# Optimization experiments

Measured on AMD Instinct MI355X. Metric: run time of the kernel, lower is better.

The kernel has to match this reference:

```python
import jax, jax.numpy as jnp
import numpy as np

LN_EPS = 1e-5

def _layernorm(x, gamma, beta):
    mu = jnp.mean(x, axis=-1, keepdims=True)
    var = jnp.var(x, axis=-1, keepdims=True)
    return (x - mu) * jax.lax.rsqrt(var + LN_EPS) * gamma + beta

def setup_inputs() -> dict:
    key = jax.random.key(0)
    ks = jax.random.split(key, 4)
    B, s, d, L = 8, 192, 512, 8
    h = 2048  # embed_dim * 2
    return {
        "lags": jax.random.normal(ks[0], (B, s, d, L), dtype=jnp.float32),
        "gamma1": jnp.ones((d,), jnp.float32),
        "beta1": jnp.zeros((d,), jnp.float32),
        "W1": jax.random.normal(ks[1], (d, h), jnp.float32) * (1.0 / np.sqrt(d)),
        "b1": jnp.zeros((h,), jnp.float32),
        "W2": jax.random.normal(ks[2], (h, d), jnp.float32) * (1.0 / np.sqrt(h)),
        "b2": jnp.zeros((d,), jnp.float32),
        "gamma3": jnp.ones((d,), jnp.float32),
        "beta3": jnp.zeros((d,), jnp.float32),
    }

def reference(lags, gamma1, beta1, W1, b1, W2, b2, gamma3, beta3):
    B, s, d, L = lags.shape
    # (B, s, d, L) -> (B, s, L, d) -> (B, S=s*L, d)
    x = jnp.transpose(lags, (0, 1, 3, 2)).reshape(B, s * L, d)
    scale = 1.0 / jnp.sqrt(jnp.asarray(d, x.dtype))
    # single-head, unprojected attention: scores = X X^T / sqrt(d)
    scores = jnp.einsum('bqd,bkd->bqk', x, x) * scale  # [B, S, S]
    attn = jax.nn.softmax(scores, axis=-1)
    attn_out = jnp.einsum('bqk,bkd->bqd', attn, x)
    q = _layernorm(x + attn_out, gamma1, beta1)
    ff = jnp.dot(jax.nn.gelu(jnp.dot(q, W1) + b1, approximate=False), W2) + b2
    out = _layernorm(q + ff, gamma3, beta3)
    # (B, S, d) -> (B, s, L, d) -> (B, s, d, L)
    return jnp.transpose(out.reshape(B, s, L, d), (0, 1, 3, 2))
```

## Files before the change

### kernel.cpp

```cpp
#include <hip/hip_runtime.h>
#include <hip/hip_bf16.h>
#include <math.h>

#define B_ 8
#define S_ 192
#define D_ 512
#define L_ 8
#define SQ 1536
#define H_ 2048
#define NROW (B_*SQ)
#define SCALE_QK 0.04419417382415922f
#define SCALE_QK2 0.06377551974755906f

typedef unsigned short ushort_t;
typedef unsigned int uint_t;
typedef __attribute__((ext_vector_type(8))) short bf16x8;
typedef __attribute__((ext_vector_type(4))) float f32x4;

__device__ __forceinline__ float bfu2f(ushort_t u) { return __uint_as_float((unsigned)u << 16); }
__device__ __forceinline__ ushort_t f2bfu(float f) {
  __hip_bfloat16 h = __float2bfloat16(f);
  return *reinterpret_cast<ushort_t*>(&h);
}

__device__ __forceinline__ float gelu_tanh(float x) {
  float x2 = x * x;
  float u2 = x * fmaf(0.0713548162f, x2, 1.5957691216f);
  float e = __expf(u2);
  float r = fmaf(-2.0f, __builtin_amdgcn_rcpf(e + 1.0f), 1.0f);
  float hx = 0.5f * x;
  return fmaf(hx, r, hx);
}

__device__ __forceinline__ void gl_lds16(const ushort_t* g, ushort_t* l) {
  __builtin_amdgcn_global_load_lds(
      (const __attribute__((address_space(1))) unsigned int*)g,
      (__attribute__((address_space(3))) unsigned int*)l, 16, 0, 0);
}

#define VMWAIT(N) asm volatile("s_waitcnt vmcnt(" #N ")" ::: "memory")

__global__ __launch_bounds__(256) void k_prep(const float* __restrict__ lags,
                                              float* __restrict__ x,
                                              ushort_t* __restrict__ x_bf,
                                              ushort_t* __restrict__ xT,
                                              float* __restrict__ rowsum,
                                              const float* __restrict__ W1,
                                              ushort_t* __restrict__ w1t,
                                              const float* __restrict__ W2,
                                              ushort_t* __restrict__ w2t) {
  __shared__ float tileF[512][9];
  __shared__ ushort_t tileW[64][65];
  const int tid = threadIdx.x;
  if (blockIdx.x < 1536) {
    const int bx = blockIdx.x;
    if (tid < 8) rowsum[(size_t)bx * 8 + tid] = 0.f;
    const float* in = lags + (size_t)bx * 4096;
    #pragma unroll
    for (int it = 0; it < 4; ++it) {
      int f = (tid + it * 256) * 4;
      float4 v = *reinterpret_cast<const float4*>(in + f);
      int k = f >> 3, l0 = f & 7;
      tileF[k][l0] = v.x; tileF[k][l0 + 1] = v.y; tileF[k][l0 + 2] = v.z; tileF[k][l0 + 3] = v.w;
    }
    __syncthreads();
    const int l = tid >> 5, kbase = tid & 31;
    const size_t r = (size_t)bx * 8 + l;
    #pragma unroll
    for (int j = 0; j < 16; ++j) {
      int k = kbase + 32 * j;
      float v = tileF[k][l];
      x[r * D_ + k] = v;
      x_bf[r * D_ + k] = f2bfu(v);
    }
    const int b = bx / S_, si = bx - b * S_;
    #pragma unroll
    for (int dd = 0; dd < 2; ++dd) {
      int d = tid + dd * 256;
      uint_t pk[4];
      #pragma unroll
      for (int j = 0; j < 4; ++j) {
        uint_t lo = f2bfu(tileF[d][2 * j]);
        uint_t hi = f2bfu(tileF[d][2 * j + 1]);
        pk[j] = (hi << 16) | lo;
      }
      uint_t* dst = (uint_t*)(xT + ((size_t)b * D_ + d) * SQ + si * 8);
      *reinterpret_cast<uint4*>(dst) = make_uint4(pk[0], pk[1], pk[2], pk[3]);
    }
  } else {
    int id = blockIdx.x - 1536;
    const float* W; ushort_t* Wt; int K, N, n0, k0;
    if (id < 256) {
      W = W1; Wt = w1t; K = D_; N = H_;
      n0 = (id & 31) * 64; k0 = (id >> 5) * 64;
    } else {
      id -= 256;
      W = W2; Wt = w2t; K = H_; N = D_;
      n0 = (id & 7) * 64; k0 = (id >> 3) * 64;
    }
    for (int i = tid; i < 4096; i += 256) {
      int kk = i >> 6, nn = i & 63;
      tileW[nn][kk] = f2bfu(W[(size_t)(k0 + kk) * N + n0 + nn]);
    }
    __syncthreads();
    for (int i = tid; i < 4096; i += 256) {
      int nn = i >> 6, kk = i & 63;
      Wt[(size_t)(n0 + nn) * K + k0 + kk] = tileW[nn][kk];
    }
  }
}

template<int MODE>
__global__ __launch_bounds__(256) void k_gemm(const ushort_t* __restrict__ A,
                                              const ushort_t* __restrict__ Bt,
                                              const float* __restrict__ bias,
                                              float* __restrict__ rsums,
                                              void* __restrict__ Cout,
                                              int M, int K, int N,
                                              size_t sAz, size_t sBz, size_t sCz,
                                              float scale) {
  A  += (size_t)blockIdx.z * sAz;
  Bt += (size_t)blockIdx.z * sBz;
  __shared__ ushort_t As0[128 * 64];
  __shared__ ushort_t As1[128 * 64];
  __shared__ ushort_t Bs0[128 * 64];
  __shared__ ushort_t Bs1[128 * 64];
  const int tid = threadIdx.x;
  int m0, n0;
  if (MODE == 6) {
    int lidx = blockIdx.x, bi = 0;
    while (lidx >= 12 - bi) { lidx -= 12 - bi; ++bi; }
    m0 = bi * 128; n0 = (bi + lidx) * 128;
  } else {
    m0 = blockIdx.y * 128; n0 = blockIdx.x * 128;
  }
  const int w = tid >> 6, lane = tid & 63;
  const int wr = w >> 1, wc = w & 1;
  const int l15 = lane & 15, quad = lane >> 4;
  const int lrow8 = lane >> 3;
  const int cg = ((lane & 7) ^ lrow8) * 8;
  const int xsw = l15 & 7;
  const int lbase = (w * 32) * 64;
  const size_t sK8 = (size_t)8 * K;

  f32x4 acc[4][4];
  if (MODE <= 1) {
    #pragma unroll
    for (int nj = 0; nj < 4; ++nj) {
      float bv = bias[n0 + wc * 64 + nj * 16 + l15];
      #pragma unroll
      for (int mi = 0; mi < 4; ++mi) acc[mi][nj] = (f32x4){bv, bv, bv, bv};
    }
  } else {
    #pragma unroll
    for (int nj = 0; nj < 4; ++nj)
      #pragma unroll
      for (int mi = 0; mi < 4; ++mi) acc[mi][nj] = (f32x4){0.f, 0.f, 0.f, 0.f};
  }

  const ushort_t* gA = A  + (size_t)(m0 + w * 32 + lrow8) * K + cg;
  const ushort_t* gB = Bt + (size_t)(n0 + w * 32 + lrow8) * K + cg;

#define STAGE(AS, BS) do {                                                  \
    ushort_t* la_ = &AS[lbase]; ushort_t* lb_ = &BS[lbase];                 \
    _Pragma("unroll")                                                       \
    for (int j_ = 0; j_ < 4; ++j_) {                                        \
      gl_lds16(gA + (size_t)j_ * sK8, la_ + j_ * 8 * 64);                   \
      gl_lds16(gB + (size_t)j_ * sK8, lb_ + j_ * 8 * 64);                   \
    }                                                                       \
    gA += 64; gB += 64;                                                     \
  } while (0)

#define COMPUTE(AS, BS) do {                                                \
    _Pragma("unroll")                                                       \
    for (int kk_ = 0; kk_ < 2; ++kk_) {                                     \
      const int csel_ = ((kk_ * 4 + quad) ^ xsw) * 8;                       \
      bf16x8 af_[4], bf_[4];                                                \
      _Pragma("unroll")                                                     \
      for (int mi_ = 0; mi_ < 4; ++mi_)                                     \
        af_[mi_] = *reinterpret_cast<const bf16x8*>(                        \
            &AS[(wr * 64 + mi_ * 16 + l15) * 64 + csel_]);                  \
      _Pragma("unroll")                                                     \
      for (int nj_ = 0; nj_ < 4; ++nj_)                                     \
        bf_[nj_] = *reinterpret_cast<const bf16x8*>(                        \
            &BS[(wc * 64 + nj_ * 16 + l15) * 64 + csel_]);                  \
      _Pragma("unroll")                                                     \
      for (int mi_ = 0; mi_ < 4; ++mi_)                                     \
        _Pragma("unroll")                                                   \
        for (int nj_ = 0; nj_ < 4; ++nj_)                                   \
          acc[mi_][nj_] = __builtin_amdgcn_mfma_f32_16x16x32_bf16(          \
              af_[mi_], bf_[nj_], acc[mi_][nj_], 0, 0, 0);                  \
    }                                                                       \
  } while (0)

  STAGE(As0, Bs0);
  STAGE(As1, Bs1);

  const int nt = K >> 6;
  for (int t = 0; t < nt - 2; t += 2) {
    VMWAIT(8);
    __builtin_amdgcn_s_barrier();
    COMPUTE(As0, Bs0);
    __builtin_amdgcn_s_barrier();
    STAGE(As0, Bs0);
    VMWAIT(8);
    __builtin_amdgcn_s_barrier();
    COMPUTE(As1, Bs1);
    __builtin_amdgcn_s_barrier();
    STAGE(As1, Bs1);
  }
  VMWAIT(8);
  __builtin_amdgcn_s_barrier();
  COMPUTE(As0, Bs0);
  VMWAIT(0);
  __builtin_amdgcn_s_barrier();
  COMPUTE(As1, Bs1);

#undef STAGE
#undef COMPUTE

  ushort_t* Cb = (ushort_t*)Cout + (size_t)blockIdx.z * sCz;
  float*    Cf = (float*)Cout    + (size_t)blockIdx.z * sCz;

  if (MODE == 6) {
    float* rs = rsums + (size_t)blockIdx.z * SQ;
    const bool offdiag = (m0 != n0);
    ushort_t* mir = (wc == 0) ? As0 : Bs0;
    float colpart[4] = {0.f, 0.f, 0.f, 0.f};
    #pragma unroll
    for (int mi = 0; mi < 4; ++mi)
      #pragma unroll
      for (int r = 0; r < 4; ++r) {
        int rl = wr * 64 + mi * 16 + quad * 4 + r;
        int gr = m0 + rl;
        float s = 0.f;
        #pragma unroll
        for (int nj = 0; nj < 4; ++nj) {
          int cl = nj * 16 + l15;
          int gc = n0 + wc * 64 + cl;
          float e = exp2f(acc[mi][nj][r] * scale);
          ushort_t ub = f2bfu(e);
          Cb[(size_t)gr * N + gc] = ub;
          if (offdiag) mir[cl * 128 + (rl ^ ((cl & 7) << 4))] = ub;
          float er = bfu2f(ub);
          s += er;
          colpart[nj] += er;
        }
        #pragma unroll
        for (int m_ = 1; m_ < 16; m_ <<= 1) s += __shfl_xor(s, m_);
        if (l15 == 0) atomicAdd(&rs[gr], s);
      }
    if (offdiag) {
      #pragma unroll
      for (int nj = 0; nj < 4; ++nj) {
        float cs = colpart[nj];
        cs += __shfl_xor(cs, 16);
        cs += __shfl_xor(cs, 32);
        if (quad == 0) atomicAdd(&rs[n0 + wc * 64 + nj * 16 + l15], cs);
      }
      __syncthreads();
      int row = tid >> 1, seg = tid & 1;
      const ushort_t* src = (row < 64) ? As0 : Bs0;
      int rl2 = row & 63;
      ushort_t* dst = &Cb[(size_t)(n0 + row) * N + m0 + seg * 64];
      #pragma unroll
      for (int h = 0; h < 4; ++h) {
        int c0 = seg * 64 + h * 16;
        int sb = rl2 * 128 + (c0 ^ ((rl2 & 7) << 4));
        uint4 v0 = *reinterpret_cast<const uint4*>(&src[sb]);
        uint4 v1 = *reinterpret_cast<const uint4*>(&src[sb + 8]);
        *reinterpret_cast<uint4*>(&dst[h * 16])     = v0;
        *reinterpret_cast<uint4*>(&dst[h * 16 + 8]) = v1;
      }
    }
  } else {
    const float* rsr = rsums + (size_t)blockIdx.z * SQ;
    #pragma unroll
    for (int mi = 0; mi < 4; ++mi)
      #pragma unroll
      for (int nj = 0; nj < 4; ++nj) {
        int gc = n0 + wc * 64 + nj * 16 + l15;
        #pragma unroll
        for (int r = 0; r < 4; ++r) {
          int gr = m0 + wr * 64 + mi * 16 + quad * 4 + r;
          float v = acc[mi][nj][r];
          if (MODE == 0) {
            Cb[(size_t)gr * N + gc] = f2bfu(gelu_tanh(v));
          } else if (MODE == 1) {
            Cf[(size_t)gr * N + gc] = v;
          } else if (MODE == 5) {
            Cf[(size_t)gr * N + gc] = v * __builtin_amdgcn_rcpf(rsr[gr]);
          } else {
            Cf[(size_t)gr * N + gc] = v;
          }
        }
      }
  }
}

__global__ __launch_bounds__(256) void k_ln1b(const float* __restrict__ x,
                                              const float* __restrict__ attn,
                                              const float* __restrict__ g,
                                              const float* __restrict__ be,
                                              ushort_t* __restrict__ qbf) {
  const int w = threadIdx.x >> 6, lane = threadIdx.x & 63;
  const size_t row = (size_t)blockIdx.x * 4 + w;
  const size_t base = row * D_ + lane * 8;
  float4 x0 = *reinterpret_cast<const float4*>(x + base);
  float4 x1 = *reinterpret_cast<const float4*>(x + base + 4);
  float4 a0 = *reinterpret_cast<const float4*>(attn + base);
  float4 a1 = *reinterpret_cast<const float4*>(attn + base + 4);
  float v[8] = {x0.x + a0.x, x0.y + a0.y, x0.z + a0.z, x0.w + a0.w,
                x1.x + a1.x, x1.y + a1.y, x1.z + a1.z, x1.w + a1.w};
  float s = 0.f, sq = 0.f;
  #pragma unroll
  for (int j = 0; j < 8; ++j) { s += v[j]; sq += v[j] * v[j]; }
  #pragma unroll
  for (int o = 32; o > 0; o >>= 1) { s += __shfl_down(s, o); sq += __shfl_down(sq, o); }
  s = __shfl(s, 0); sq = __shfl(sq, 0);
  float mean = s * (1.0f / 512.0f);
  float var = sq * (1.0f / 512.0f) - mean * mean;
  float rstd = rsqrtf(var + 1e-5f);
  const int kb = lane * 8;
  float4 g0 = *reinterpret_cast<const float4*>(g + kb);
  float4 g1 = *reinterpret_cast<const float4*>(g + kb + 4);
  float4 b0 = *reinterpret_cast<const float4*>(be + kb);
  float4 b1 = *reinterpret_cast<const float4*>(be + kb + 4);
  float gv[8] = {g0.x, g0.y, g0.z, g0.w, g1.x, g1.y, g1.z, g1.w};
  float bv[8] = {b0.x, b0.y, b0.z, b0.w, b1.x, b1.y, b1.z, b1.w};
  uint_t u[4];
  #pragma unroll
  for (int p = 0; p < 4; ++p) {
    uint_t lo = f2bfu((v[2*p]   - mean) * rstd * gv[2*p]   + bv[2*p]);
    uint_t hi = f2bfu((v[2*p+1] - mean) * rstd * gv[2*p+1] + bv[2*p+1]);
    u[p] = (hi << 16) | lo;
  }
  *reinterpret_cast<uint4*>(qbf + base) = make_uint4(u[0], u[1], u[2], u[3]);
}

__global__ __launch_bounds__(256) void k_ln3_f(const float* __restrict__ y,
                                               const ushort_t* __restrict__ qbf,
                                               const float* __restrict__ g3,
                                               const float* __restrict__ be3,
                                               float* __restrict__ out) {
  __shared__ float ynorm[8][512];
  const int tid = threadIdx.x;
  const int w = tid >> 6, lane = tid & 63;
  const int kb = lane * 8;
  #pragma unroll
  for (int rr = 0; rr < 2; ++rr) {
    int l = 2 * w + rr;
    size_t t = (size_t)blockIdx.x * 8 + l;
    size_t base = t * D_ + kb;
    float4 y0 = *reinterpret_cast<const float4*>(y + base);
    float4 y1 = *reinterpret_cast<const float4*>(y + base + 4);
    uint4 q = *reinterpret_cast<const uint4*>(qbf + base);
    float v[8];
    v[0] = y0.x + __uint_as_float(q.x << 16);
    v[1] = y0.y + __uint_as_float(q.x & 0xffff0000u);
    v[2] = y0.z + __uint_as_float(q.y << 16);
    v[3] = y0.w + __uint_as_float(q.y & 0xffff0000u);
    v[4] = y1.x + __uint_as_float(q.z << 16);
    v[5] = y1.y + __uint_as_float(q.z & 0xffff0000u);
    v[6] = y1.z + __uint_as_float(q.w << 16);
    v[7] = y1.w + __uint_as_float(q.w & 0xffff0000u);
    float s = 0.f, sq = 0.f;
    #pragma unroll
    for (int j = 0; j < 8; ++j) { s += v[j]; sq += v[j] * v[j]; }
    #pragma unroll
    for (int o = 32; o > 0; o >>= 1) { s += __shfl_down(s, o); sq += __shfl_down(sq, o); }
    s = __shfl(s, 0); sq = __shfl(sq, 0);
    float mean = s * (1.0f / 512.0f);
    float var = sq * (1.0f / 512.0f) - mean * mean;
    float rstd = rsqrtf(var + 1e-5f);
    float4 g0 = *reinterpret_cast<const float4*>(g3 + kb);
    float4 g1 = *reinterpret_cast<const float4*>(g3 + kb + 4);
    float4 b0 = *reinterpret_cast<const float4*>(be3 + kb);
    float4 b1 = *reinterpret_cast<const float4*>(be3 + kb + 4);
    float gv[8] = {g0.x, g0.y, g0.z, g0.w, g1.x, g1.y, g1.z, g1.w};
    float bv[8] = {b0.x, b0.y, b0.z, b0.w, b1.x, b1.y, b1.z, b1.w};
    #pragma unroll
    for (int j = 0; j < 8; ++j)
      ynorm[l][kb + j] = (v[j] - mean) * rstd * gv[j] + bv[j];
  }
  __syncthreads();
  float* ob = out + (size_t)blockIdx.x * 4096;
  #pragma unroll
  for (int kk = 0; kk < 2; ++kk) {
    int k = tid * 2 + kk;
    float4 lo = make_float4(ynorm[0][k], ynorm[1][k], ynorm[2][k], ynorm[3][k]);
    float4 hi = make_float4(ynorm[4][k], ynorm[5][k], ynorm[6][k], ynorm[7][k]);
    *reinterpret_cast<float4*>(ob + (size_t)k * 8)     = lo;
    *reinterpret_cast<float4*>(ob + (size_t)k * 8 + 4) = hi;
  }
}

#define TS 64
#define KT 16
__global__ __launch_bounds__(256) void k_build_x_s(const float* __restrict__ lags,
                                                   float* __restrict__ x, int b_base) {
  int idx = blockIdx.x * 256 + threadIdx.x;
  int k = idx & (D_ - 1);
  int r = idx >> 9;
  int b = b_base + r / SQ;
  int t = r - (r / SQ) * SQ;
  int si = t >> 3, l = t & 7;
  size_t src = (((size_t)(b * S_ + si) * D_ + k) << 3) + l;
  x[idx] = lags[src];
}

__global__ __launch_bounds__(256) void k_scores(const float* __restrict__ x,
                                                float* __restrict__ sc, int b_base) {
  const float* A = x;
  float* C = sc;
  __shared__ float As[TS][KT + 1];
  __shared__ float Bs[TS][KT + 1];
  int tx = threadIdx.x & 15, ty = threadIdx.x >> 4;
  int j0 = blockIdx.x * TS, i0 = blockIdx.y * TS;
  float acc[4][4] = {};
  int lk = threadIdx.x & 15, lr = threadIdx.x >> 4;
  for (int k0 = 0; k0 < D_; k0 += KT) {
    #pragma unroll
    for (int it = 0; it < 4; ++it) {
      As[lr + 16 * it][lk] = A[(size_t)(i0 + lr + 16 * it) * D_ + k0 + lk];
      Bs[lr + 16 * it][lk] = A[(size_t)(j0 + lr + 16 * it) * D_ + k0 + lk];
    }
    __syncthreads();
    #pragma unroll
    for (int kk = 0; kk < KT; ++kk) {
      float a[4], bb[4];
      #pragma unroll
      for (int r = 0; r < 4; ++r) a[r] = As[ty * 4 + r][kk];
      #pragma unroll
      for (int c = 0; c < 4; ++c) bb[c] = Bs[tx * 4 + c][kk];
      #pragma unroll
      for (int r = 0; r < 4; ++r)
        #pragma unroll
        for (int c = 0; c < 4; ++c) acc[r][c] = fmaf(a[r], bb[c], acc[r][c]);
    }
    __syncthreads();
  }
  #pragma unroll
  for (int r = 0; r < 4; ++r) {
    float4 v = make_float4(acc[r][0]*SCALE_QK, acc[r][1]*SCALE_QK,
                           acc[r][2]*SCALE_QK, acc[r][3]*SCALE_QK);
    *reinterpret_cast<float4*>(&C[(size_t)(i0 + ty*4 + r) * SQ + j0 + tx*4]) = v;
  }
}

__global__ __launch_bounds__(256) void k_softmax(float* __restrict__ sc) {
  float* row = sc + (size_t)blockIdx.x * SQ;
  int tid = threadIdx.x;
  __shared__ float red[8];
  float m = -1e30f;
  for (int j = tid; j < SQ; j += 256) m = fmaxf(m, row[j]);
  #pragma unroll
  for (int o = 32; o > 0; o >>= 1) m = fmaxf(m, __shfl_down(m, o));
  if ((tid & 63) == 0) red[tid >> 6] = m;
  __syncthreads();
  m = fmaxf(fmaxf(red[0], red[1]), fmaxf(red[2], red[3]));
  __syncthreads();
  float ssum = 0.f;
  for (int j = tid; j < SQ; j += 256) { float e = expf(row[j] - m); row[j] = e; ssum += e; }
  #pragma unroll
  for (int o = 32; o > 0; o >>= 1) ssum += __shfl_down(ssum, o);
  if ((tid & 63) == 0) red[4 + (tid >> 6)] = ssum;
  __syncthreads();
  float inv = 1.0f / (red[4] + red[5] + red[6] + red[7]);
  for (int j = tid; j < SQ; j += 256) row[j] *= inv;
}

__global__ __launch_bounds__(256) void k_attn(const float* __restrict__ x,
                                              const float* __restrict__ sc,
                                              float* __restrict__ attn) {
  const float* X = x;
  const float* P = sc;
  float* O = attn;
  __shared__ float Ps[TS][KT + 1];
  __shared__ float Xs[KT][TS];
  int tx = threadIdx.x & 15, ty = threadIdx.x >> 4;
  int j0 = blockIdx.x * TS, i0 = blockIdx.y * TS;
  float acc[4][4] = {};
  int lk = threadIdx.x & 15, lr = threadIdx.x >> 4;
  int lc = threadIdx.x & 63, lrow = threadIdx.x >> 6;
  for (int k0 = 0; k0 < SQ; k0 += KT) {
    #pragma unroll
    for (int it = 0; it < 4; ++it)
      Ps[lr + 16 * it][lk] = P[(size_t)(i0 + lr + 16 * it) * SQ + k0 + lk];
    #pragma unroll
    for (int it = 0; it < 4; ++it)
      Xs[lrow + 4 * it][lc] = X[(size_t)(k0 + lrow + 4 * it) * D_ + j0 + lc];
    __syncthreads();
    #pragma unroll
    for (int kk = 0; kk < KT; ++kk) {
      float a[4], bb[4];
      #pragma unroll
      for (int r = 0; r < 4; ++r) a[r] = Ps[ty * 4 + r][kk];
      #pragma unroll
      for (int c = 0; c < 4; ++c) bb[c] = Xs[kk][tx * 4 + c];
      #pragma unroll
      for (int r = 0; r < 4; ++r)
        #pragma unroll
        for (int c = 0; c < 4; ++c) acc[r][c] = fmaf(a[r], bb[c], acc[r][c]);
    }
    __syncthreads();
  }
  #pragma unroll
  for (int r = 0; r < 4; ++r) {
    float4 v = make_float4(acc[r][0], acc[r][1], acc[r][2], acc[r][3]);
    *reinterpret_cast<float4*>(&O[(size_t)(i0 + ty*4 + r) * D_ + j0 + tx*4]) = v;
  }
}

__global__ __launch_bounds__(256) void k_ln1(const float* __restrict__ x,
                                             const float* __restrict__ attn,
                                             const float* __restrict__ g,
                                             const float* __restrict__ be,
                                             float* __restrict__ qout) {
  size_t base = (size_t)blockIdx.x * D_;
  int tid = threadIdx.x;
  __shared__ float rl[8];
  float v0 = x[base + tid] + attn[base + tid];
  float v1 = x[base + tid + 256] + attn[base + tid + 256];
  float s = v0 + v1, sq = v0 * v0 + v1 * v1;
  #pragma unroll
  for (int o = 32; o > 0; o >>= 1) { s += __shfl_down(s, o); sq += __shfl_down(sq, o); }
  int lane = tid & 63, wid = tid >> 6;
  if (lane == 0) { rl[wid] = s; rl[4 + wid] = sq; }
  __syncthreads();
  s = rl[0] + rl[1] + rl[2] + rl[3];
  sq = rl[4] + rl[5] + rl[6] + rl[7];
  float mean = s * (1.0f / 512.0f);
  float var = sq * (1.0f / 512.0f) - mean * mean;
  float rstd = rsqrtf(var + 1e-5f);
  qout[base + tid]       = (v0 - mean) * rstd * g[tid] + be[tid];
  qout[base + tid + 256] = (v1 - mean) * rstd * g[tid + 256] + be[tid + 256];
}

__global__ __launch_bounds__(256, 2) void k_ffn(
    const float* __restrict__ q,
    const float* __restrict__ W1, const float* __restrict__ b1,
    const float* __restrict__ W2, const float* __restrict__ b2,
    const float* __restrict__ g3, const float* __restrict__ be3,
    float* __restrict__ out, int row_base)
{
  __shared__ float qs[8][D_];
  __shared__ float mid[8][H_];
  const int tid = threadIdx.x;
  const int row0 = blockIdx.x * 8;
  for (int idx = tid; idx < 8 * D_; idx += 256)
    qs[idx >> 9][idx & (D_ - 1)] = q[(size_t)row0 * D_ + idx];
  __syncthreads();
  float acc[8][8];
  {
    float4 bA = *reinterpret_cast<const float4*>(b1 + (tid << 3));
    float4 bB = *reinterpret_cast<const float4*>(b1 + (tid << 3) + 4);
    float bv[8] = {bA.x, bA.y, bA.z, bA.w, bB.x, bB.y, bB.z, bB.w};
    #pragma unroll
    for (int jj = 0; jj < 8; ++jj)
      #pragma unroll
      for (int r = 0; r < 8; ++r) acc[jj][r] = bv[jj];
  }
  for (int k4 = 0; k4 < D_ / 4; ++k4) {
    float4 qv[8];
    #pragma unroll
    for (int r = 0; r < 8; ++r)
      qv[r] = *reinterpret_cast<const float4*>(&qs[r][k4 << 2]);
    #pragma unroll
    for (int kk = 0; kk < 4; ++kk) {
      const int k = (k4 << 2) + kk;
      float4 wA = *reinterpret_cast<const float4*>(W1 + (size_t)k * H_ + (tid << 3));
      float4 wB = *reinterpret_cast<const float4*>(W1 + (size_t)k * H_ + (tid << 3) + 4);
      float wv[8] = {wA.x, wA.y, wA.z, wA.w, wB.x, wB.y, wB.z, wB.w};
      #pragma unroll
      for (int r = 0; r < 8; ++r) {
        float qk = (kk == 0) ? qv[r].x : (kk == 1) ? qv[r].y : (kk == 2) ? qv[r].z : qv[r].w;
        #pragma unroll
        for (int jj = 0; jj < 8; ++jj) acc[jj][r] = fmaf(qk, wv[jj], acc[jj][r]);
      }
    }
  }
  #pragma unroll
  for (int jj = 0; jj < 8; ++jj)
    #pragma unroll
    for (int r = 0; r < 8; ++r) {
      float v = acc[jj][r];
      mid[r][(tid << 3) + jj] = 0.5f * v * (1.0f + erff(v * 0.70710678118654752f));
    }
  __syncthreads();
  float acc2[8][2];
  {
    float b20 = b2[tid << 1], b21 = b2[(tid << 1) + 1];
    #pragma unroll
    for (int r = 0; r < 8; ++r) { acc2[r][0] = b20; acc2[r][1] = b21; }
  }
  for (int j4 = 0; j4 < H_ / 4; ++j4) {
    float4 mv[8];
    #pragma unroll
    for (int r = 0; r < 8; ++r)
      mv[r] = *reinterpret_cast<const float4*>(&mid[r][j4 << 2]);
    #pragma unroll
    for (int kk = 0; kk < 4; ++kk) {
      const int j = (j4 << 2) + kk;
      float2 wv = *reinterpret_cast<const float2*>(W2 + (size_t)j * D_ + (tid << 1));
      #pragma unroll
      for (int r = 0; r < 8; ++r) {
        float m = (kk == 0) ? mv[r].x : (kk == 1) ? mv[r].y : (kk == 2) ? mv[r].z : mv[r].w;
        acc2[r][0] = fmaf(m, wv.x, acc2[r][0]);
        acc2[r][1] = fmaf(m, wv.y, acc2[r][1]);
      }
    }
  }
  __syncthreads();
  float* ys = &mid[0][0];
  #pragma unroll
  for (int r = 0; r < 8; ++r) {
    ys[r * D_ + (tid << 1)]     = qs[r][(tid << 1)]     + acc2[r][0];
    ys[r * D_ + (tid << 1) + 1] = qs[r][(tid << 1) + 1] + acc2[r][1];
  }
  __syncthreads();
  float g3a = g3[tid],  g3b = g3[tid + 256];
  float be3a = be3[tid], be3b = be3[tid + 256];
  float* rl = &qs[0][0];
  for (int r = 0; r < 8; ++r) {
    float v0 = ys[r * D_ + tid], v1 = ys[r * D_ + tid + 256];
    float s = v0 + v1, sq = v0 * v0 + v1 * v1;
    #pragma unroll
    for (int o = 32; o > 0; o >>= 1) { s += __shfl_down(s, o); sq += __shfl_down(sq, o); }
    int lane = tid & 63, wid = tid >> 6;
    if (lane == 0) { rl[wid] = s; rl[4 + wid] = sq; }
    __syncthreads();
    s = rl[0] + rl[1] + rl[2] + rl[3];
    sq = rl[4] + rl[5] + rl[6] + rl[7];
    __syncthreads();
    float mean = s * (1.0f / 512.0f);
    float var = sq * (1.0f / 512.0f) - mean * mean;
    float rstd = rsqrtf(var + 1e-5f);
    int t = row_base + row0 + r;
    int b = t / SQ, tt = t - b * SQ;
    int si = tt >> 3, l = tt & 7;
    size_t ob = (((size_t)(b * S_ + si) * D_) << 3) + l;
    out[ob + ((size_t)tid << 3)]         = (v0 - mean) * rstd * g3a + be3a;
    out[ob + ((size_t)(tid + 256) << 3)] = (v1 - mean) * rstd * g3b + be3b;
  }
}

extern "C" void kernel_launch(void* const* d_in, const int* in_sizes, int n_in,
                              void* d_out, int out_size, void* d_ws, size_t ws_size,
                              hipStream_t stream) {
  const float* lags   = (const float*)d_in[0];
  const float* gamma1 = (const float*)d_in[1];
  const float* beta1  = (const float*)d_in[2];
  const float* W1     = (const float*)d_in[3];
  const float* b1     = (const float*)d_in[4];
  const float* W2     = (const float*)d_in[5];
  const float* b2     = (const float*)d_in[6];
  const float* g3     = (const float*)d_in[7];
  const float* be3    = (const float*)d_in[8];
  float* out = (float*)d_out;

  float* ws = (float*)d_ws;
  const size_t NX  = (size_t)B_ * SQ * D_;
  const size_t NXB = (size_t)SQ * D_;
  const size_t NS  = (size_t)SQ * SQ;

  const size_t need_full = (3 * NX + 8 * NS) * sizeof(float);

  if (ws_size >= need_full) {
    float* x        = ws;
    float* attn     = x + NX;
    ushort_t* q_bf  = (ushort_t*)(attn + NX);
    ushort_t* w1t   = q_bf + NX;
    ushort_t* w2t   = w1t + (size_t)H_ * D_;
    float* rowsum   = (float*)(w2t + (size_t)H_ * D_);
    ushort_t* region = (ushort_t*)(rowsum + (size_t)B_ * SQ);
    ushort_t* sc_bf = region;
    ushort_t* x_bf  = region + 8 * NS;
    ushort_t* xT_bf = x_bf + NX;
    ushort_t* mid_bf = region;

    k_prep<<<dim3(2048), 256, 0, stream>>>(lags, x, x_bf, xT_bf, rowsum,
                                           W1, w1t, W2, w2t);
    k_gemm<6><<<dim3(78, 1, B_), 256, 0, stream>>>(
        x_bf, x_bf, nullptr, rowsum, sc_bf, SQ, D_, SQ, NXB, NXB, NS, SCALE_QK2);
    k_gemm<5><<<dim3(D_ / 128, SQ / 128, B_), 256, 0, stream>>>(
        sc_bf, xT_bf, nullptr, rowsum, attn, SQ, SQ, D_, NS, NXB, NXB, 1.0f);
    k_ln1b<<<dim3(NROW / 4), 256, 0, stream>>>(x, attn, gamma1, beta1, q_bf);
    k_gemm<0><<<dim3(H_ / 128, NROW / 128, 1), 256, 0, stream>>>(
        q_bf, w1t, b1, nullptr, mid_bf, NROW, D_, H_, 0, 0, 0, 1.0f);
    k_gemm<1><<<dim3(D_ / 128, NROW / 128, 1), 256, 0, stream>>>(
        mid_bf, w2t, b2, nullptr, attn, NROW, H_, D_, 0, 0, 0, 1.0f);
    k_ln3_f<<<dim3(B_ * S_), 256, 0, stream>>>(attn, q_bf, g3, be3, out);
  } else {
    float* xb   = ws;
    float* sc   = xb + NXB;
    float* atb  = sc + NS;
    float* qb   = atb + NXB;
    for (int b = 0; b < B_; ++b) {
      k_build_x_s<<<dim3((unsigned)(NXB / 256)), 256, 0, stream>>>(lags, xb, b);
      k_scores<<<dim3(SQ / TS, SQ / TS, 1), 256, 0, stream>>>(xb, sc, b);
      k_softmax<<<dim3(SQ, 1, 1), 256, 0, stream>>>(sc);
      k_attn<<<dim3(D_ / TS, SQ / TS, 1), 256, 0, stream>>>(xb, sc, atb);
      k_ln1<<<dim3(SQ), 256, 0, stream>>>(xb, atb, gamma1, beta1, qb);
      k_ffn<<<dim3(SQ / 8), 256, 0, stream>>>(qb, W1, b1, W2, b2, g3, be3, out, b * SQ);
    }
  }
}
```

Measured before the change: 278.6 us.

## Add K=32 tiled GEMM kernel for attention-value and FFN matmuls

Adds a new GEMM kernel that stages 32-wide K slices instead of 64, halving LDS use per block (32 KB vs 64 KB) and using a different XOR swizzle. The attention-value and both FFN GEMMs switch to it, while the original kernel is reduced to the symmetric score-only path. The aim is higher occupancy from the smaller shared-memory footprint. The cost is twice as many barrier and pipeline iterations per K, with less MFMA work between synchronisations.

```diff
diff --git a/kernel.cpp b/kernel.cpp
--- a/kernel.cpp
+++ b/kernel.cpp
@@ -111,9 +111,125 @@
 }
 
 template<int MODE>
+__global__ __launch_bounds__(256) void k_gemm32(const ushort_t* __restrict__ A,
+                                                const ushort_t* __restrict__ Bt,
+                                                const float* __restrict__ bias,
+                                                const float* __restrict__ rsums,
+                                                void* __restrict__ Cout,
+                                                int M, int K, int N,
+                                                size_t sAz, size_t sBz, size_t sCz) {
+  A  += (size_t)blockIdx.z * sAz;
+  Bt += (size_t)blockIdx.z * sBz;
+  __shared__ ushort_t As0[128 * 32];
+  __shared__ ushort_t As1[128 * 32];
+  __shared__ ushort_t Bs0[128 * 32];
+  __shared__ ushort_t Bs1[128 * 32];
+  const int tid = threadIdx.x;
+  const int m0 = blockIdx.y * 128, n0 = blockIdx.x * 128;
+  const int w = tid >> 6, lane = tid & 63;
+  const int wr = w >> 1, wc = w & 1;
+  const int l15 = lane & 15, quad = lane >> 4;
+  const int cg = ((lane & 3) ^ ((lane >> 3) & 3)) * 8;
+  const int csel = (quad ^ ((l15 >> 1) & 3)) * 8;
+  const int lbase = w * 1024;
+  const size_t sK16 = (size_t)16 * K;
+
+  f32x4 acc[4][4];
+  if (MODE <= 1) {
+    #pragma unroll
+    for (int nj = 0; nj < 4; ++nj) {
+      float bv = bias[n0 + wc * 64 + nj * 16 + l15];
+      #pragma unroll
+      for (int mi = 0; mi < 4; ++mi) acc[mi][nj] = (f32x4){bv, bv, bv, bv};
+    }
+  } else {
+    #pragma unroll
+    for (int nj = 0; nj < 4; ++nj)
+      #pragma unroll
+      for (int mi = 0; mi < 4; ++mi) acc[mi][nj] = (f32x4){0.f, 0.f, 0.f, 0.f};
+  }
+
+  const ushort_t* gA = A  + (size_t)(m0 + w * 32 + (lane >> 2)) * K + cg;
+  const ushort_t* gB = Bt + (size_t)(n0 + w * 32 + (lane >> 2)) * K + cg;
+
+#define STAGE32(AS, BS) do {                                                \
+    gl_lds16(gA,        &AS[lbase]);                                        \
+    gl_lds16(gA + sK16, &AS[lbase + 512]);                                  \
+    gl_lds16(gB,        &BS[lbase]);                                        \
+    gl_lds16(gB + sK16, &BS[lbase + 512]);                                  \
+    gA += 32; gB += 32;                                                     \
+  } while (0)
+
+#define COMPUTE32(AS, BS) do {                                              \
+    bf16x8 af_[4], bf_[4];                                                  \
+    _Pragma("unroll")                                                       \
+    for (int mi_ = 0; mi_ < 4; ++mi_)                                       \
+      af_[mi_] = *reinterpret_cast<const bf16x8*>(                          \
+          &AS[(wr * 64 + mi_ * 16 + l15) * 32 + csel]);                     \
+    _Pragma("unroll")                                                       \
+    for (int nj_ = 0; nj_ < 4; ++nj_)                                       \
+      bf_[nj_] = *reinterpret_cast<const bf16x8*>(                          \
+          &BS[(wc * 64 + nj_ * 16 + l15) * 32 + csel]);                     \
+    _Pragma("unroll")                                                       \
+    for (int mi_ = 0; mi_ < 4; ++mi_)                                       \
+      _Pragma("unroll")                                                     \
+      for (int nj_ = 0; nj_ < 4; ++nj_)                                     \
+        acc[mi_][nj_] = __builtin_amdgcn_mfma_f32_16x16x32_bf16(            \
+            af_[mi_], bf_[nj_], acc[mi_][nj_], 0, 0, 0);                    \
+  } while (0)
+
+  STAGE32(As0, Bs0);
+  STAGE32(As1, Bs1);
+
+  const int nt = K >> 5;
+  for (int t = 0; t < nt - 2; t += 2) {
+    VMWAIT(4);
+    __builtin_amdgcn_s_barrier();
+    COMPUTE32(As0, Bs0);
+    __builtin_amdgcn_s_barrier();
+    STAGE32(As0, Bs0);
+    VMWAIT(4);
+    __builtin_amdgcn_s_barrier();
+    COMPUTE32(As1, Bs1);
+    __builtin_amdgcn_s_barrier();
+    STAGE32(As1, Bs1);
+  }
+  VMWAIT(4);
+  __builtin_amdgcn_s_barrier();
+  COMPUTE32(As0, Bs0);
+  VMWAIT(0);
+  __builtin_amdgcn_s_barrier();
+  COMPUTE32(As1, Bs1);
+
+#undef STAGE32
+#undef COMPUTE32
+
+  ushort_t* Cb = (ushort_t*)Cout + (size_t)blockIdx.z * sCz;
+  float*    Cf = (float*)Cout    + (size_t)blockIdx.z * sCz;
+  const float* rsr = rsums + (size_t)blockIdx.z * SQ;
+  #pragma unroll
+  for (int mi = 0; mi < 4; ++mi)
+    #pragma unroll
+    for (int nj = 0; nj < 4; ++nj) {
+      int gc = n0 + wc * 64 + nj * 16 + l15;
+      #pragma unroll
+      for (int r = 0; r < 4; ++r) {
+        int gr = m0 + wr * 64 + mi * 16 + quad * 4 + r;
+        float v = acc[mi][nj][r];
+        if (MODE == 0) {
+          Cb[(size_t)gr * N + gc] = f2bfu(gelu_tanh(v));
+        } else if (MODE == 1) {
+          Cf[(size_t)gr * N + gc] = v;
+        } else {
+          Cf[(size_t)gr * N + gc] = v * __builtin_amdgcn_rcpf(rsr[gr]);
+        }
+      }
+    }
+}
+
+template<int MODE>
 __global__ __launch_bounds__(256) void k_gemm(const ushort_t* __restrict__ A,
                                               const ushort_t* __restrict__ Bt,
-                                              const float* __restrict__ bias,
                                               float* __restrict__ rsums,
                                               void* __restrict__ Cout,
                                               int M, int K, int N,
@@ -127,12 +243,10 @@
   __shared__ ushort_t Bs1[128 * 64];
   const int tid = threadIdx.x;
   int m0, n0;
-  if (MODE == 6) {
+  {
     int lidx = blockIdx.x, bi = 0;
     while (lidx >= 12 - bi) { lidx -= 12 - bi; ++bi; }
     m0 = bi * 128; n0 = (bi + lidx) * 128;
-  } else {
-    m0 = blockIdx.y * 128; n0 = blockIdx.x * 128;
   }
   const int w = tid >> 6, lane = tid & 63;
   const int wr = w >> 1, wc = w & 1;
@@ -144,19 +258,10 @@
   const size_t sK8 = (size_t)8 * K;
 
   f32x4 acc[4][4];
-  if (MODE <= 1) {
-    #pragma unroll
-    for (int nj = 0; nj < 4; ++nj) {
-      float bv = bias[n0 + wc * 64 + nj * 16 + l15];
-      #pragma unroll
-      for (int mi = 0; mi < 4; ++mi) acc[mi][nj] = (f32x4){bv, bv, bv, bv};
-    }
-  } else {
-    #pragma unroll
-    for (int nj = 0; nj < 4; ++nj)
-      #pragma unroll
-      for (int mi = 0; mi < 4; ++mi) acc[mi][nj] = (f32x4){0.f, 0.f, 0.f, 0.f};
-  }
+  #pragma unroll
+  for (int nj = 0; nj < 4; ++nj)
+    #pragma unroll
+    for (int mi = 0; mi < 4; ++mi) acc[mi][nj] = (f32x4){0.f, 0.f, 0.f, 0.f};
 
   const ushort_t* gA = A  + (size_t)(m0 + w * 32 + lrow8) * K + cg;
   const ushort_t* gB = Bt + (size_t)(n0 + w * 32 + lrow8) * K + cg;
@@ -220,81 +325,56 @@
 #undef COMPUTE
 
   ushort_t* Cb = (ushort_t*)Cout + (size_t)blockIdx.z * sCz;
-  float*    Cf = (float*)Cout    + (size_t)blockIdx.z * sCz;
-
-  if (MODE == 6) {
-    float* rs = rsums + (size_t)blockIdx.z * SQ;
-    const bool offdiag = (m0 != n0);
-    ushort_t* mir = (wc == 0) ? As0 : Bs0;
-    float colpart[4] = {0.f, 0.f, 0.f, 0.f};
-    #pragma unroll
-    for (int mi = 0; mi < 4; ++mi)
-      #pragma unroll
-      for (int r = 0; r < 4; ++r) {
-        int rl = wr * 64 + mi * 16 + quad * 4 + r;
-        int gr = m0 + rl;
-        float s = 0.f;
-        #pragma unroll
-        for (int nj = 0; nj < 4; ++nj) {
-          int cl = nj * 16 + l15;
-          int gc = n0 + wc * 64 + cl;
-          float e = exp2f(acc[mi][nj][r] * scale);
-          ushort_t ub = f2bfu(e);
-          Cb[(size_t)gr * N + gc] = ub;
-          if (offdiag) mir[cl * 128 + (rl ^ ((cl & 7) << 4))] = ub;
-          float er = bfu2f(ub);
-          s += er;
-          colpart[nj] += er;
-        }
-        #pragma unroll
-        for (int m_ = 1; m_ < 16; m_ <<= 1) s += __shfl_xor(s, m_);
-        if (l15 == 0) atomicAdd(&rs[gr], s);
+
+  float* rs = rsums + (size_t)blockIdx.z * SQ;
+  const bool offdiag = (m0 != n0);
+  ushort_t* mir = (wc == 0) ? As0 : Bs0;
+  float colpart[4] = {0.f, 0.f, 0.f, 0.f};
+  #pragma unroll
+  for (int mi = 0; mi < 4; ++mi)
+    #pragma unroll
+    for (int r = 0; r < 4; ++r) {
+      int rl = wr * 64 + mi * 16 + quad * 4 + r;
+      int gr = m0 + rl;
+      float s = 0.f;
+      #pragma unroll
+      for (int nj = 0; nj < 4; ++nj) {
+        int cl = nj * 16 + l15;
+        int gc = n0 + wc * 64 + cl;
+        float e = exp2f(acc[mi][nj][r] * scale);
+        ushort_t ub = f2bfu(e);
+        Cb[(size_t)gr * N + gc] = ub;
+        if (offdiag) mir[cl * 128 + (rl ^ ((cl & 7) << 4))] = ub;
+        float er = bfu2f(ub);
+        s += er;
+        colpart[nj] += er;
       }
-    if (offdiag) {
-      #pragma unroll
-      for (int nj = 0; nj < 4; ++nj) {
-        float cs = colpart[nj];
-        cs += __shfl_xor(cs, 16);
-        cs += __shfl_xor(cs, 32);
-        if (quad == 0) atomicAdd(&rs[n0 + wc * 64 + nj * 16 + l15], cs);
-      }
-      __syncthreads();
-      int row = tid >> 1, seg = tid & 1;
-      const ushort_t* src = (row < 64) ? As0 : Bs0;
-      int rl2 = row & 63;
-      ushort_t* dst = &Cb[(size_t)(n0 + row) * N + m0 + seg * 64];
-      #pragma unroll
-      for (int h = 0; h < 4; ++h) {
-        int c0 = seg * 64 + h * 16;
-        int sb = rl2 * 128 + (c0 ^ ((rl2 & 7) << 4));
-        uint4 v0 = *reinterpret_cast<const uint4*>(&src[sb]);
-        uint4 v1 = *reinterpret_cast<const uint4*>(&src[sb + 8]);
-        *reinterpret_cast<uint4*>(&dst[h * 16])     = v0;
-        *reinterpret_cast<uint4*>(&dst[h * 16 + 8]) = v1;
-      }
-    }
-  } else {
-    const float* rsr = rsums + (size_t)blockIdx.z * SQ;
-    #pragma unroll
-    for (int mi = 0; mi < 4; ++mi)
-      #pragma unroll
-      for (int nj = 0; nj < 4; ++nj) {
-        int gc = n0 + wc * 64 + nj * 16 + l15;
-        #pragma unroll
-        for (int r = 0; r < 4; ++r) {
-          int gr = m0 + wr * 64 + mi * 16 + quad * 4 + r;
-          float v = acc[mi][nj][r];
-          if (MODE == 0) {
-            Cb[(size_t)gr * N + gc] = f2bfu(gelu_tanh(v));
-          } else if (MODE == 1) {
-            Cf[(size_t)gr * N + gc] = v;
-          } else if (MODE == 5) {
-            Cf[(size_t)gr * N + gc] = v * __builtin_amdgcn_rcpf(rsr[gr]);
-          } else {
-            Cf[(size_t)gr * N + gc] = v;
-          }
-        }
-      }
+      #pragma unroll
+      for (int m_ = 1; m_ < 16; m_ <<= 1) s += __shfl_xor(s, m_);
+      if (l15 == 0) atomicAdd(&rs[gr], s);
+    }
+  if (offdiag) {
+    #pragma unroll
+    for (int nj = 0; nj < 4; ++nj) {
+      float cs = colpart[nj];
+      cs += __shfl_xor(cs, 16);
+      cs += __shfl_xor(cs, 32);
+      if (quad == 0) atomicAdd(&rs[n0 + wc * 64 + nj * 16 + l15], cs);
+    }
+    __syncthreads();
+    int row = tid >> 1, seg = tid & 1;
+    const ushort_t* src = (row < 64) ? As0 : Bs0;
+    int rl2 = row & 63;
+    ushort_t* dst = &Cb[(size_t)(n0 + row) * N + m0 + seg * 64];
+    #pragma unroll
+    for (int h = 0; h < 4; ++h) {
+      int c0 = seg * 64 + h * 16;
+      int sb = rl2 * 128 + (c0 ^ ((rl2 & 7) << 4));
+      uint4 v0 = *reinterpret_cast<const uint4*>(&src[sb]);
+      uint4 v1 = *reinterpret_cast<const uint4*>(&src[sb + 8]);
+      *reinterpret_cast<uint4*>(&dst[h * 16])     = v0;
+      *reinterpret_cast<uint4*>(&dst[h * 16 + 8]) = v1;
+    }
   }
 }
 
@@ -682,14 +762,14 @@
     k_prep<<<dim3(2048), 256, 0, stream>>>(lags, x, x_bf, xT_bf, rowsum,
                                            W1, w1t, W2, w2t);
     k_gemm<6><<<dim3(78, 1, B_), 256, 0, stream>>>(
-        x_bf, x_bf, nullptr, rowsum, sc_bf, SQ, D_, SQ, NXB, NXB, NS, SCALE_QK2);
-    k_gemm<5><<<dim3(D_ / 128, SQ / 128, B_), 256, 0, stream>>>(
-        sc_bf, xT_bf, nullptr, rowsum, attn, SQ, SQ, D_, NS, NXB, NXB, 1.0f);
+        x_bf, x_bf, rowsum, sc_bf, SQ, D_, SQ, NXB, NXB, NS, SCALE_QK2);
+    k_gemm32<5><<<dim3(D_ / 128, SQ / 128, B_), 256, 0, stream>>>(
+        sc_bf, xT_bf, nullptr, rowsum, attn, SQ, SQ, D_, NS, NXB, NXB);
     k_ln1b<<<dim3(NROW / 4), 256, 0, stream>>>(x, attn, gamma1, beta1, q_bf);
-    k_gemm<0><<<dim3(H_ / 128, NROW / 128, 1), 256, 0, stream>>>(
-        q_bf, w1t, b1, nullptr, mid_bf, NROW, D_, H_, 0, 0, 0, 1.0f);
-    k_gemm<1><<<dim3(D_ / 128, NROW / 128, 1), 256, 0, stream>>>(
-        mid_bf, w2t, b2, nullptr, attn, NROW, H_, D_, 0, 0, 0, 1.0f);
+    k_gemm32<0><<<dim3(H_ / 128, NROW / 128, 1), 256, 0, stream>>>(
+        q_bf, w1t, b1, nullptr, mid_bf, NROW, D_, H_, 0, 0, 0);
+    k_gemm32<1><<<dim3(D_ / 128, NROW / 128, 1), 256, 0, stream>>>(
+        mid_bf, w2t, b2, nullptr, attn, NROW, H_, D_, 0, 0, 0);
     k_ln3_f<<<dim3(B_ * S_), 256, 0, stream>>>(attn, q_bf, g3, be3, out);
   } else {
     float* xb   = ws;
```

Measured after the change: 291.6 us. +4.7%, slower.
